# Kernel tuning notes

Measured on AMD Instinct MI355X. Metric: run time of the kernel, lower is better.

Reference implementation:

```python
import jax, jax.numpy as jnp
import numpy as np

B, L, T = 256, 1024, 128

def setup_inputs() -> dict:
    key = jax.random.key(0)
    k1, k2, k3, k4 = jax.random.split(key, 4)
    inputs = jax.random.normal(k1, (B, L, T), dtype=jnp.float32)
    tag_indices = jax.random.randint(k2, (B, L), 0, T, dtype=jnp.int64)
    sequence_lengths = jax.random.randint(k3, (B,), 1, L + 1, dtype=jnp.int64)
    # xavier-ish scale for transitions
    transition_params = jax.random.normal(k4, (T, T), dtype=jnp.float32) * (2.0 / (T + T)) ** 0.5
    return {"inputs": inputs, "tag_indices": tag_indices,
            "sequence_lengths": sequence_lengths, "transition_params": transition_params}

def _crf_log_likelihood(inputs, tag_indices, sequence_lengths, transition_params):
    b, l, t = inputs.shape
    mask = (jnp.arange(l)[None, :] < sequence_lengths[:, None]).astype(inputs.dtype)  # [B,L]

    # --- unary score: sum_t inputs[b, t, tag[b,t]] over valid t ---
    unary = jnp.take_along_axis(inputs, tag_indices[:, :, None], axis=2)[:, :, 0]  # [B,L]
    unary_score = jnp.sum(unary * mask, axis=1)

    # --- binary score: sum_t trans[tag[t], tag[t+1]] masked by mask[:,1:] ---
    trans_sc = transition_params[tag_indices[:, :-1], tag_indices[:, 1:]]  # [B,L-1]
    binary_score = jnp.sum(trans_sc * mask[:, 1:], axis=1)
    sequence_scores = unary_score + binary_score

    # --- log normalizer via forward algorithm (log-space scan) ---
    first = inputs[:, 0]                               # [B,T]
    rest = jnp.transpose(inputs[:, 1:], (1, 0, 2))     # [L-1,B,T]

    def step(state, inp_t):
        # state: [B,T] previous alphas; transition broadcast: [B,T_prev,T_next]
        new = inp_t + jax.nn.logsumexp(state[:, :, None] + transition_params[None], axis=1)
        return new, new

    _, alphas = jax.lax.scan(step, first, rest)        # [L-1,B,T]
    # original indexes all_alphas at max(0, seq_len - 2)
    idx = jnp.clip(sequence_lengths - 2, 0, l - 2)
    final_alphas = alphas[idx, jnp.arange(b)]          # [B,T]
    log_norm = jax.nn.logsumexp(final_alphas, axis=1)
    log_norm = jnp.where(sequence_lengths <= 0, jnp.zeros_like(log_norm), log_norm)

    return sequence_scores - log_norm

def reference(inputs, tag_indices, sequence_lengths, transition_params):
    return _crf_log_likelihood(inputs, tag_indices, sequence_lengths, transition_params)
```

## Files before the change

kernel.cpp:

```cpp
#include <hip/hip_runtime.h>


#define B_   256
#define LL   1024
#define TT   128
#define NBLK 16
#define L2E  1.4426950408889634f
#define LN2f 0.6931471805599453f

typedef __attribute__((ext_vector_type(8))) short bf16x8;
typedef __attribute__((ext_vector_type(4))) float f32x4;
union bfrw { unsigned w[4]; bf16x8 v; };

__device__ __forceinline__ unsigned bfround(float x) {
    unsigned u = __float_as_uint(x);
    return u + 0x7fffu + ((u >> 16) & 1u);
}
__device__ __forceinline__ unsigned pack2(float lo, float hi) {
#if __has_builtin(__builtin_amdgcn_cvt_pk_bf16_f32)
    auto p = __builtin_amdgcn_cvt_pk_bf16_f32(lo, hi);
    unsigned w; __builtin_memcpy(&w, &p, 4); return w;
#else
    return __builtin_amdgcn_perm(bfround(hi), bfround(lo), 0x07060302);
#endif
}
__device__ __forceinline__ void lds_barrier() {
    asm volatile("s_waitcnt lgkmcnt(0)\n\ts_barrier" ::: "memory");
}


template<bool FWD, int PH>
__device__ __forceinline__ void phase(int t, float& Dacc,
                                      float4 (&up)[4][2],
                                      const bf16x8 (&af)[2][4],
                                      bf16x8& bs,
                                      short* fset, float* sb2,
                                      const float* pu,
                                      float* cl, float* dc,
                                      int o0, int o1, int o2, int ws,
                                      int cb, int tfin, int W4, int q, int b)
{
    constexpr int CUR  = PH & 1;
    constexpr int NXT  = CUR ^ 1;
    constexpr int SLOT = FWD ? ((1 + PH) & 3) : ((3 - PH) & 3);

    bf16x8 bo0 = *(const bf16x8*)(fset + CUR * 2048 + o0);
    bf16x8 bo1 = *(const bf16x8*)(fset + CUR * 2048 + o1);
    bf16x8 bo2 = *(const bf16x8*)(fset + CUR * 2048 + o2);
    float sprev = sb2[CUR * 16 + b];

    f32x4 ae0, ae1, ao0, ao1;
    ae0 = __builtin_amdgcn_mfma_f32_16x16x32_bf16(af[0][0], bs,  (f32x4){0.f,0.f,0.f,0.f}, 0, 0, 0);
    ae1 = __builtin_amdgcn_mfma_f32_16x16x32_bf16(af[1][0], bs,  (f32x4){0.f,0.f,0.f,0.f}, 0, 0, 0);
    ao0 = __builtin_amdgcn_mfma_f32_16x16x32_bf16(af[0][1], bo0, (f32x4){0.f,0.f,0.f,0.f}, 0, 0, 0);
    ao1 = __builtin_amdgcn_mfma_f32_16x16x32_bf16(af[1][1], bo0, (f32x4){0.f,0.f,0.f,0.f}, 0, 0, 0);
    ae0 = __builtin_amdgcn_mfma_f32_16x16x32_bf16(af[0][2], bo1, ae0, 0, 0, 0);
    ae1 = __builtin_amdgcn_mfma_f32_16x16x32_bf16(af[1][2], bo1, ae1, 0, 0, 0);
    ao0 = __builtin_amdgcn_mfma_f32_16x16x32_bf16(af[0][3], bo2, ao0, 0, 0, 0);
    ao1 = __builtin_amdgcn_mfma_f32_16x16x32_bf16(af[1][3], bo2, ao1, 0, 0, 0);

    float ex[2][4];
    #pragma unroll
    for (int m = 0; m < 2; ++m) {
        float4 v = up[SLOT][m];
        ex[m][0] = __builtin_amdgcn_exp2f(v.x * L2E);
        ex[m][1] = __builtin_amdgcn_exp2f(v.y * L2E);
        ex[m][2] = __builtin_amdgcn_exp2f(v.z * L2E);
        ex[m][3] = __builtin_amdgcn_exp2f(v.w * L2E);
    }
    {
        int tp = FWD ? (t + 4) : (t - 5);
        tp = tp < 0 ? 0 : (tp > LL - 1 ? LL - 1 : tp);
        const float* pt = pu + (size_t)tp * TT;
        up[SLOT][0] = *(const float4*)(pt);
        up[SLOT][1] = *(const float4*)(pt + 16);
    }

    float ci = __builtin_amdgcn_rcpf(sprev);
    float lg = __builtin_amdgcn_logf(sprev);
    bool inj = (!FWD) && (tfin == t - 1);
    float cis  = inj ? 0.f : ci;
    float injf = inj ? 1.f : 0.f;
    Dacc = inj ? 0.f : (Dacc + lg);

    f32x4 a0 = ae0 + ao0;
    f32x4 a1 = ae1 + ao1;

    float rv[2][4];
    #pragma unroll
    for (int r = 0; r < 4; ++r) {
        rv[0][r] = cis * a0[r] + injf;
        rv[1][r] = cis * a1[r] + injf;
    }

    if (!FWD) {
        bool cap = (cb == t - 1) && (cb != tfin);
        if (__any(cap)) {
            if (cap) {
                float4 c0 = {rv[0][0], rv[0][1], rv[0][2], rv[0][3]};
                float4 c1 = {rv[1][0], rv[1][1], rv[1][2], rv[1][3]};
                *(float4*)(cl + b * TT + 32 * W4 + q * 4)      = c0;
                *(float4*)(cl + b * TT + 32 * W4 + 16 + q * 4) = c1;
                if (W4 == 0 && q == 0) dc[b] = Dacc;
            }
        }
    }

    float ov[2][4];
    #pragma unroll
    for (int r = 0; r < 4; ++r) {
        ov[0][r] = ex[0][r] * rv[0][r];
        ov[1][r] = ex[1][r] * rv[1][r];
    }

    if (FWD) {
        bool cap = (cb == t);
        if (__any(cap)) {
            if (cap) {
                float4 c0 = {ov[0][0], ov[0][1], ov[0][2], ov[0][3]};
                float4 c1 = {ov[1][0], ov[1][1], ov[1][2], ov[1][3]};
                *(float4*)(cl + b * TT + 32 * W4 + q * 4)      = c0;
                *(float4*)(cl + b * TT + 32 * W4 + 16 + q * 4) = c1;
                if (W4 == 0 && q == 0) dc[b] = Dacc;
            }
        }
    }

    if (W4 == 0 && q == 0) sb2[NXT * 16 + b] = a0[0];

    bfrw pk;
    pk.w[0] = pack2(ov[0][0], ov[0][1]);
    pk.w[1] = pack2(ov[0][2], ov[0][3]);
    pk.w[2] = pack2(ov[1][0], ov[1][1]);
    pk.w[3] = pack2(ov[1][2], ov[1][3]);
    bs = pk.v;
    *(bf16x8*)(fset + NXT * 2048 + ws) = pk.v;

    lds_barrier();
}

__launch_bounds__(512, 1)
__global__ void crf_scan(const float* __restrict__ inputs,
                         const int*   __restrict__ tags,
                         const int*   __restrict__ slens,
                         const float* __restrict__ trans,
                         float* __restrict__ qcap, float* __restrict__ rcap,
                         float* __restrict__ dqv,  float* __restrict__ drv,
                         int* __restrict__ perm, float* __restrict__ scorebuf)
{
    __shared__ __align__(16) short fragls[2][2][4][64 * 8];
    __shared__ __align__(16) float capl[2][16][TT];
    __shared__ float dcap[2][16];
    __shared__ float sbuf[2][2][16];
    __shared__ float ssb[8];
    __shared__ int keys[B_];

    const int tid = threadIdx.x;

    if (blockIdx.x >= NBLK) {
        const int sbid = blockIdx.x - NBLK;
        const int lane = tid & 63, w = tid >> 6;
        #pragma unroll 1
        for (int bi = 0; bi < 4; ++bi) {
            const int b = sbid * 4 + bi;
            const int slen = slens[b];
            const float* inb  = inputs + (size_t)b * LL * TT;
            const int*   tagb = tags + b * LL;
            float sc = 0.f;
            for (int t = tid; t < slen; t += 512) {
                int tg = tagb[t];
                float v = inb[(size_t)t * TT + tg];
                if (t >= 1) v += trans[tagb[t - 1] * TT + tg];
                sc += v;
            }
            #pragma unroll
            for (int off = 32; off > 0; off >>= 1) sc += __shfl_xor(sc, off, 64);
            if (lane == 0) ssb[w] = sc;
            __syncthreads();
            if (tid == 0) scorebuf[b] = ssb[0] + ssb[1] + ssb[2] + ssb[3]
                                      + ssb[4] + ssb[5] + ssb[6] + ssb[7];
            __syncthreads();
        }
        return;
    }

    const int g = blockIdx.x;

    if (tid < 256) keys[tid] = slens[tid] * 256 + tid;
    __syncthreads();
    for (int k = 2; k <= B_; k <<= 1) {
        for (int s = k >> 1; s > 0; s >>= 1) {
            if (tid < 256) {
                int ixj = tid ^ s;
                if (ixj > tid) {
                    int a = keys[tid], b2 = keys[ixj];
                    bool asc = ((tid & k) == 0);
                    if ((a > b2) == asc) { keys[tid] = b2; keys[ixj] = a; }
                }
            }
            __syncthreads();
        }
    }
    if (tid < 16) perm[g * 16 + tid] = keys[g * 16 + tid] & 255;

    const int set  = tid >> 8;
    const bool isf = (set == 0);
    const int lane = tid & 63;
    const int W4   = __builtin_amdgcn_readfirstlane((tid >> 6) & 3);
    const int q    = lane >> 4;
    const int b    = lane & 15;

    const int key = keys[g * 16 + b];
    const int ob  = key & 255;
    const int sl  = key >> 8;
    int tfin = sl - 1; if (tfin < 1) tfin = 1;

    int tmax = tfin;
    #pragma unroll
    for (int o = 1; o < 16; o <<= 1) {
        int c2 = __shfl_xor(tmax, o, 16); tmax = c2 > tmax ? c2 : tmax;
    }
    tmax = __builtin_amdgcn_readfirstlane(tmax);

    const int C  = (tmax + 4) >> 1;
    const int cb = tfin < C ? tfin : C;

    int cmax = cb, cmin = cb;
    #pragma unroll
    for (int o = 1; o < 16; o <<= 1) {
        int a = __shfl_xor(cmax, o, 16); cmax = a > cmax ? a : cmax;
        int b2 = __shfl_xor(cmin, o, 16); cmin = b2 < cmin ? b2 : cmin;
    }
    cmax = __builtin_amdgcn_readfirstlane(cmax);
    cmin = __builtin_amdgcn_readfirstlane(cmin);

    const int tb0 = (tmax + 4) & ~3;
    const int nif = (cmax + 3) >> 2;
    const int nib = (tb0 - cmin + 3) >> 2;
    const int NS  = nif > nib ? nif : nib;

    const int c1 = (W4 == 0) ? 1 : 0;
    const int c2 = (W4 <= 1) ? 2 : 1;
    const int c3 = (W4 <= 2) ? 3 : 2;
    const int o0 = (c1 * 64 + lane) * 8;
    const int o1 = (c2 * 64 + lane) * 8;
    const int o2 = (c3 * 64 + lane) * 8;
    const int ws = (W4 * 64 + lane) * 8;

    bf16x8 af[2][4];
    #pragma unroll
    for (int m = 0; m < 2; ++m) {
        const int j = 32 * W4 + 16 * m + b;
        #pragma unroll
        for (int i = 0; i < 4; ++i) {
            const int c = (i == 0) ? W4 : (i == 1) ? c1 : (i == 2) ? c2 : c3;
            #pragma unroll
            for (int jj = 0; jj < 8; ++jj) {
                int k = 32 * c + 16 * (jj >> 2) + 4 * q + (jj & 3);
                int idx = isf ? (k * TT + j) : (j * TT + k);
                float ev = __builtin_amdgcn_exp2f(trans[idx] * L2E);
                af[m][i][jj] = (short)(bfround(ev) >> 16);
            }
        }
    }

    short* fset = &fragls[set][0][0][0];
    float* sb2  = &sbuf[set][0][0];
    float* cl   = &capl[set][0][0];
    float* dc   = &dcap[set][0];

    const float* pu = inputs + (size_t)ob * LL * TT + 32 * W4 + q * 4;
    float Dacc = 0.f;
    float4 up[4][2];
    bf16x8 bs;

    if (W4 == 0 && lane < 16) sb2[lane] = 1.0f;

    if (isf) {
        float q0[2][4];
        #pragma unroll
        for (int m = 0; m < 2; ++m) {
            float4 v = *(const float4*)(pu + m * 16);
            q0[m][0] = __builtin_amdgcn_exp2f(v.x * L2E);
            q0[m][1] = __builtin_amdgcn_exp2f(v.y * L2E);
            q0[m][2] = __builtin_amdgcn_exp2f(v.z * L2E);
            q0[m][3] = __builtin_amdgcn_exp2f(v.w * L2E);
        }
        bfrw pk;
        pk.w[0] = pack2(q0[0][0], q0[0][1]);
        pk.w[1] = pack2(q0[0][2], q0[0][3]);
        pk.w[2] = pack2(q0[1][0], q0[1][1]);
        pk.w[3] = pack2(q0[1][2], q0[1][3]);
        bs = pk.v;
        *(bf16x8*)(fset + ws) = pk.v;

        #pragma unroll
        for (int s = 1; s <= 4; ++s) {
            up[s & 3][0] = *(const float4*)(pu + (size_t)s * TT);
            up[s & 3][1] = *(const float4*)(pu + (size_t)s * TT + 16);
        }
    } else {
        bfrw pk;
        pk.w[0] = pk.w[1] = pk.w[2] = pk.w[3] = 0x3F803F80u;
        bs = pk.v;
        *(bf16x8*)(fset + ws) = pk.v;
        if (cb == tfin) {
            float4 one4 = {1.f, 1.f, 1.f, 1.f};
            *(float4*)(cl + b * TT + 32 * W4 + q * 4)      = one4;
            *(float4*)(cl + b * TT + 32 * W4 + 16 + q * 4) = one4;
            if (W4 == 0 && q == 0) dc[b] = 0.f;
        }
        #pragma unroll
        for (int ph = 0; ph < 4; ++ph) {
            int ui = tb0 - 1 - ph;
            ui = ui > LL - 1 ? LL - 1 : (ui < 0 ? 0 : ui);
            up[(3 - ph) & 3][0] = *(const float4*)(pu + (size_t)ui * TT);
            up[(3 - ph) & 3][1] = *(const float4*)(pu + (size_t)ui * TT + 16);
        }
    }
    __syncthreads();

    if (isf) {
        for (int i = 0; i < NS; ++i) {
            const int tb = 1 + 4 * i;
            phase<true,0>(tb+0, Dacc, up, af, bs, fset, sb2, pu, cl, dc, o0,o1,o2,ws, cb, tfin, W4, q, b);
            phase<true,1>(tb+1, Dacc, up, af, bs, fset, sb2, pu, cl, dc, o0,o1,o2,ws, cb, tfin, W4, q, b);
            phase<true,2>(tb+2, Dacc, up, af, bs, fset, sb2, pu, cl, dc, o0,o1,o2,ws, cb, tfin, W4, q, b);
            phase<true,3>(tb+3, Dacc, up, af, bs, fset, sb2, pu, cl, dc, o0,o1,o2,ws, cb, tfin, W4, q, b);
        }
    } else {
        for (int i = 0; i < NS; ++i) {
            const int tb = tb0 - 4 * i;
            phase<false,0>(tb-0, Dacc, up, af, bs, fset, sb2, pu, cl, dc, o0,o1,o2,ws, cb, tfin, W4, q, b);
            phase<false,1>(tb-1, Dacc, up, af, bs, fset, sb2, pu, cl, dc, o0,o1,o2,ws, cb, tfin, W4, q, b);
            phase<false,2>(tb-2, Dacc, up, af, bs, fset, sb2, pu, cl, dc, o0,o1,o2,ws, cb, tfin, W4, q, b);
            phase<false,3>(tb-3, Dacc, up, af, bs, fset, sb2, pu, cl, dc, o0,o1,o2,ws, cb, tfin, W4, q, b);
        }
    }

    float* gout = isf ? qcap : rcap;
    const int ltid = tid & 255;
    #pragma unroll
    for (int i = 0; i < 2; ++i) {
        float4 v = *(const float4*)(cl + i * 1024 + ltid * 4);
        *(float4*)(gout + (size_t)g * 16 * TT + i * 1024 + ltid * 4) = v;
    }
    if (ltid < 16) (isf ? dqv : drv)[g * 16 + ltid] = dc[ltid];
}

__global__ void crf_comb(const float* __restrict__ qcap, const float* __restrict__ rcap,
                         const float* __restrict__ dqv, const float* __restrict__ drv,
                         const int* __restrict__ perm, const float* __restrict__ scorebuf,
                         float* __restrict__ out) {
    const int tid = threadIdx.x;
    const int r16 = tid >> 4, part = tid & 15;
    const int rank = blockIdx.x * 16 + r16;
    const float* qc = qcap + rank * TT + part * 8;
    const float* rc = rcap + rank * TT + part * 8;
    float4 a0 = *(const float4*)(qc);
    float4 a1 = *(const float4*)(qc + 4);
    float4 b0 = *(const float4*)(rc);
    float4 b1 = *(const float4*)(rc + 4);
    float s = a0.x*b0.x + a0.y*b0.y + a0.z*b0.z + a0.w*b0.w
            + a1.x*b1.x + a1.y*b1.y + a1.z*b1.z + a1.w*b1.w;
    #pragma unroll
    for (int o = 1; o < 16; o <<= 1) s += __shfl_xor(s, o, 16);
    if (part == 0) {
        int ob = perm[rank];
        float logZ = LN2f * (__builtin_amdgcn_logf(s) + dqv[rank] + drv[rank]);
        out[ob] = scorebuf[ob] - logZ;
    }
}

extern "C" void kernel_launch(void* const* d_in, const int* in_sizes, int n_in,
                              void* d_out, int out_size, void* d_ws, size_t ws_size,
                              hipStream_t stream) {
    const float* inputs = (const float*)d_in[0];
    const int*   tags   = (const int*)d_in[1];
    const int*   slens  = (const int*)d_in[2];
    const float* trans  = (const float*)d_in[3];
    float* out = (float*)d_out;

    float* qcap = (float*)d_ws;
    float* rcap = qcap + 32768;
    float* dqv  = rcap + 32768;
    float* drv  = dqv + 256;
    int*   perm = (int*)(drv + 256);
    float* scorebuf = (float*)(perm + 256);

    crf_scan<<<NBLK + 64, 512, 0, stream>>>(inputs, tags, slens, trans,
                                            qcap, rcap, dqv, drv, perm, scorebuf);
    crf_comb<<<NBLK, 256, 0, stream>>>(qcap, rcap, dqv, drv, perm, scorebuf, out);
}
```

Before: 465.9 us.

## Replace per-step block barriers with per-direction LDS counter flag synchronization

Swaps the workgroup-wide s_barrier after every scan step for per-wave LDS step counters. Each wave publishes its step number and spins until the other three waves of the same direction reach the previous step. This decouples the forward and backward halves of the block, so each runs only its own step count (nif or nib) instead of the common maximum. The risks are spin-polling overhead and memory-ordering hazards: the double-buffered fragments are guarded only by waits on the previous step, so a fast wave may overwrite a buffer a slower wave is still reading.

```diff
diff --git a/kernel.cpp b/kernel.cpp
--- a/kernel.cpp
+++ b/kernel.cpp
@@ -24,25 +24,38 @@
     return __builtin_amdgcn_perm(bfround(hi), bfround(lo), 0x07060302);
 #endif
 }
-__device__ __forceinline__ void lds_barrier() {
-    asm volatile("s_waitcnt lgkmcnt(0)\n\ts_barrier" ::: "memory");
-}
 
 
 template<bool FWD, int PH>
-__device__ __forceinline__ void phase(int t, float& Dacc,
+__device__ __forceinline__ void phase(int t, int s, float& Dacc,
                                       float4 (&up)[4][2],
                                       const bf16x8 (&af)[2][4],
                                       bf16x8& bs,
-                                      short* fset, float* sb2,
+                                      short* fset, float* sb2, int* cnts,
+                                      int4& cpre,
                                       const float* pu,
                                       float* cl, float* dc,
                                       int o0, int o1, int o2, int ws,
-                                      int cb, int tfin, int W4, int q, int b)
+                                      int cb, int tfin, int W4, int q, int b,
+                                      int lane)
 {
     constexpr int CUR  = PH & 1;
     constexpr int NXT  = CUR ^ 1;
     constexpr int SLOT = FWD ? ((1 + PH) & 3) : ((3 - PH) & 3);
+
+    {
+        const int need = s - 1;
+        int mn0 = cpre.x < cpre.y ? cpre.x : cpre.y;
+        int mn1 = cpre.z < cpre.w ? cpre.z : cpre.w;
+        int mn  = mn0 < mn1 ? mn0 : mn1;
+        while (mn < need) {
+            volatile const int* vc = (volatile const int*)cnts;
+            int a0 = vc[0], a1 = vc[1], a2 = vc[2], a3 = vc[3];
+            mn0 = a0 < a1 ? a0 : a1;
+            mn1 = a2 < a3 ? a2 : a3;
+            mn  = mn0 < mn1 ? mn0 : mn1;
+        }
+    }
 
     bf16x8 bo0 = *(const bf16x8*)(fset + CUR * 2048 + o0);
     bf16x8 bo1 = *(const bf16x8*)(fset + CUR * 2048 + o1);
@@ -136,7 +149,12 @@
     bs = pk.v;
     *(bf16x8*)(fset + NXT * 2048 + ws) = pk.v;
 
-    lds_barrier();
+    asm volatile("s_waitcnt lgkmcnt(0)" ::: "memory");
+    if (lane == 0) *(volatile int*)(cnts + W4) = s;
+    {
+        volatile const int* vc = (volatile const int*)cnts;
+        cpre.x = vc[0]; cpre.y = vc[1]; cpre.z = vc[2]; cpre.w = vc[3];
+    }
 }
 
 __launch_bounds__(512, 1)
@@ -150,6 +168,7 @@
 {
     __shared__ __align__(16) short fragls[2][2][4][64 * 8];
     __shared__ __align__(16) float capl[2][16][TT];
+    __shared__ __align__(16) int cnt[2][4];
     __shared__ float dcap[2][16];
     __shared__ float sbuf[2][2][16];
     __shared__ float ssb[8];
@@ -187,6 +206,7 @@
     const int g = blockIdx.x;
 
     if (tid < 256) keys[tid] = slens[tid] * 256 + tid;
+    if (tid < 8) cnt[tid >> 2][tid & 3] = 0;
     __syncthreads();
     for (int k = 2; k <= B_; k <<= 1) {
         for (int s = k >> 1; s > 0; s >>= 1) {
@@ -237,7 +257,6 @@
     const int tb0 = (tmax + 4) & ~3;
     const int nif = (cmax + 3) >> 2;
     const int nib = (tb0 - cmin + 3) >> 2;
-    const int NS  = nif > nib ? nif : nib;
 
     const int c1 = (W4 == 0) ? 1 : 0;
     const int c2 = (W4 <= 1) ? 2 : 1;
@@ -268,11 +287,13 @@
     float* sb2  = &sbuf[set][0][0];
     float* cl   = &capl[set][0][0];
     float* dc   = &dcap[set][0];
+    int*   cnts = &cnt[set][0];
 
     const float* pu = inputs + (size_t)ob * LL * TT + 32 * W4 + q * 4;
     float Dacc = 0.f;
     float4 up[4][2];
     bf16x8 bs;
+    int4 cpre = {0, 0, 0, 0};
 
     if (W4 == 0 && lane < 16) sb2[lane] = 1.0f;
 
@@ -321,22 +342,25 @@
     __syncthreads();
 
     if (isf) {
-        for (int i = 0; i < NS; ++i) {
+        for (int i = 0; i < nif; ++i) {
             const int tb = 1 + 4 * i;
-            phase<true,0>(tb+0, Dacc, up, af, bs, fset, sb2, pu, cl, dc, o0,o1,o2,ws, cb, tfin, W4, q, b);
-            phase<true,1>(tb+1, Dacc, up, af, bs, fset, sb2, pu, cl, dc, o0,o1,o2,ws, cb, tfin, W4, q, b);
-            phase<true,2>(tb+2, Dacc, up, af, bs, fset, sb2, pu, cl, dc, o0,o1,o2,ws, cb, tfin, W4, q, b);
-            phase<true,3>(tb+3, Dacc, up, af, bs, fset, sb2, pu, cl, dc, o0,o1,o2,ws, cb, tfin, W4, q, b);
+            phase<true,0>(tb+0, tb+0, Dacc, up, af, bs, fset, sb2, cnts, cpre, pu, cl, dc, o0,o1,o2,ws, cb, tfin, W4, q, b, lane);
+            phase<true,1>(tb+1, tb+1, Dacc, up, af, bs, fset, sb2, cnts, cpre, pu, cl, dc, o0,o1,o2,ws, cb, tfin, W4, q, b, lane);
+            phase<true,2>(tb+2, tb+2, Dacc, up, af, bs, fset, sb2, cnts, cpre, pu, cl, dc, o0,o1,o2,ws, cb, tfin, W4, q, b, lane);
+            phase<true,3>(tb+3, tb+3, Dacc, up, af, bs, fset, sb2, cnts, cpre, pu, cl, dc, o0,o1,o2,ws, cb, tfin, W4, q, b, lane);
         }
     } else {
-        for (int i = 0; i < NS; ++i) {
+        for (int i = 0; i < nib; ++i) {
             const int tb = tb0 - 4 * i;
-            phase<false,0>(tb-0, Dacc, up, af, bs, fset, sb2, pu, cl, dc, o0,o1,o2,ws, cb, tfin, W4, q, b);
-            phase<false,1>(tb-1, Dacc, up, af, bs, fset, sb2, pu, cl, dc, o0,o1,o2,ws, cb, tfin, W4, q, b);
-            phase<false,2>(tb-2, Dacc, up, af, bs, fset, sb2, pu, cl, dc, o0,o1,o2,ws, cb, tfin, W4, q, b);
-            phase<false,3>(tb-3, Dacc, up, af, bs, fset, sb2, pu, cl, dc, o0,o1,o2,ws, cb, tfin, W4, q, b);
-        }
-    }
+            const int s0 = 4 * i + 1;
+            phase<false,0>(tb-0, s0+0, Dacc, up, af, bs, fset, sb2, cnts, cpre, pu, cl, dc, o0,o1,o2,ws, cb, tfin, W4, q, b, lane);
+            phase<false,1>(tb-1, s0+1, Dacc, up, af, bs, fset, sb2, cnts, cpre, pu, cl, dc, o0,o1,o2,ws, cb, tfin, W4, q, b, lane);
+            phase<false,2>(tb-2, s0+2, Dacc, up, af, bs, fset, sb2, cnts, cpre, pu, cl, dc, o0,o1,o2,ws, cb, tfin, W4, q, b, lane);
+            phase<false,3>(tb-3, s0+3, Dacc, up, af, bs, fset, sb2, cnts, cpre, pu, cl, dc, o0,o1,o2,ws, cb, tfin, W4, q, b, lane);
+        }
+    }
+
+    __syncthreads();
 
     float* gout = isf ? qcap : rcap;
     const int ltid = tid & 255;
```

New measurement: 567.6 us. 21.8% more time.

## Split forward and backward scan sets into separate 256-thread blocks

Applied to the files above, without the earlier changes.

The forward and backward half-scans used to share one 512-thread block with a shared LDS barrier. They now run as separate 256-thread blocks, twice as many, each with its own loop bound (cmax for forward, cmin for backward) instead of a common NS. This removes the coupling where each half waited at barriers for the other and ran extra iterations to match the longer half. The cost is a duplicated slen sort in every block and more blocks to launch.

```diff
diff --git a/kernel.cpp b/kernel.cpp
--- a/kernel.cpp
+++ b/kernel.cpp
@@ -34,20 +34,20 @@
                                       float4 (&up)[4][2],
                                       const bf16x8 (&af)[2][4],
                                       bf16x8& bs,
-                                      short* fset, float* sb2,
+                                      short* fragls, float* sbuf,
                                       const float* pu,
-                                      float* cl, float* dc,
+                                      float* capl, float* dcap,
                                       int o0, int o1, int o2, int ws,
-                                      int cb, int tfin, int W4, int q, int b)
+                                      int cb, int tfin, int W, int q, int b)
 {
     constexpr int CUR  = PH & 1;
     constexpr int NXT  = CUR ^ 1;
     constexpr int SLOT = FWD ? ((1 + PH) & 3) : ((3 - PH) & 3);
 
-    bf16x8 bo0 = *(const bf16x8*)(fset + CUR * 2048 + o0);
-    bf16x8 bo1 = *(const bf16x8*)(fset + CUR * 2048 + o1);
-    bf16x8 bo2 = *(const bf16x8*)(fset + CUR * 2048 + o2);
-    float sprev = sb2[CUR * 16 + b];
+    bf16x8 bo0 = *(const bf16x8*)(fragls + CUR * 2048 + o0);
+    bf16x8 bo1 = *(const bf16x8*)(fragls + CUR * 2048 + o1);
+    bf16x8 bo2 = *(const bf16x8*)(fragls + CUR * 2048 + o2);
+    float sprev = sbuf[CUR * 16 + b];
 
     f32x4 ae0, ae1, ao0, ao1;
     ae0 = __builtin_amdgcn_mfma_f32_16x16x32_bf16(af[0][0], bs,  (f32x4){0.f,0.f,0.f,0.f}, 0, 0, 0);
@@ -99,9 +99,9 @@
             if (cap) {
                 float4 c0 = {rv[0][0], rv[0][1], rv[0][2], rv[0][3]};
                 float4 c1 = {rv[1][0], rv[1][1], rv[1][2], rv[1][3]};
-                *(float4*)(cl + b * TT + 32 * W4 + q * 4)      = c0;
-                *(float4*)(cl + b * TT + 32 * W4 + 16 + q * 4) = c1;
-                if (W4 == 0 && q == 0) dc[b] = Dacc;
+                *(float4*)(capl + b * TT + 32 * W + q * 4)      = c0;
+                *(float4*)(capl + b * TT + 32 * W + 16 + q * 4) = c1;
+                if (W == 0 && q == 0) dcap[b] = Dacc;
             }
         }
     }
@@ -119,14 +119,14 @@
             if (cap) {
                 float4 c0 = {ov[0][0], ov[0][1], ov[0][2], ov[0][3]};
                 float4 c1 = {ov[1][0], ov[1][1], ov[1][2], ov[1][3]};
-                *(float4*)(cl + b * TT + 32 * W4 + q * 4)      = c0;
-                *(float4*)(cl + b * TT + 32 * W4 + 16 + q * 4) = c1;
-                if (W4 == 0 && q == 0) dc[b] = Dacc;
-            }
-        }
-    }
-
-    if (W4 == 0 && q == 0) sb2[NXT * 16 + b] = a0[0];
+                *(float4*)(capl + b * TT + 32 * W + q * 4)      = c0;
+                *(float4*)(capl + b * TT + 32 * W + 16 + q * 4) = c1;
+                if (W == 0 && q == 0) dcap[b] = Dacc;
+            }
+        }
+    }
+
+    if (W == 0 && q == 0) sbuf[NXT * 16 + b] = a0[0];
 
     bfrw pk;
     pk.w[0] = pack2(ov[0][0], ov[0][1]);
@@ -134,12 +134,12 @@
     pk.w[2] = pack2(ov[1][0], ov[1][1]);
     pk.w[3] = pack2(ov[1][2], ov[1][3]);
     bs = pk.v;
-    *(bf16x8*)(fset + NXT * 2048 + ws) = pk.v;
+    *(bf16x8*)(fragls + NXT * 2048 + ws) = pk.v;
 
     lds_barrier();
 }
 
-__launch_bounds__(512, 1)
+__launch_bounds__(256, 1)
 __global__ void crf_scan(const float* __restrict__ inputs,
                          const int*   __restrict__ tags,
                          const int*   __restrict__ slens,
@@ -148,17 +148,17 @@
                          float* __restrict__ dqv,  float* __restrict__ drv,
                          int* __restrict__ perm, float* __restrict__ scorebuf)
 {
-    __shared__ __align__(16) short fragls[2][2][4][64 * 8];
-    __shared__ __align__(16) float capl[2][16][TT];
-    __shared__ float dcap[2][16];
-    __shared__ float sbuf[2][2][16];
-    __shared__ float ssb[8];
+    __shared__ __align__(16) short fragls[2 * 4 * 64 * 8];
+    __shared__ __align__(16) float capl[16 * TT];
+    __shared__ float dcap[16];
+    __shared__ float sbuf[2 * 16];
+    __shared__ float ssb[4];
     __shared__ int keys[B_];
 
     const int tid = threadIdx.x;
 
-    if (blockIdx.x >= NBLK) {
-        const int sbid = blockIdx.x - NBLK;
+    if (blockIdx.x >= 2 * NBLK) {
+        const int sbid = blockIdx.x - 2 * NBLK;
         const int lane = tid & 63, w = tid >> 6;
         #pragma unroll 1
         for (int bi = 0; bi < 4; ++bi) {
@@ -167,7 +167,7 @@
             const float* inb  = inputs + (size_t)b * LL * TT;
             const int*   tagb = tags + b * LL;
             float sc = 0.f;
-            for (int t = tid; t < slen; t += 512) {
+            for (int t = tid; t < slen; t += 256) {
                 int tg = tagb[t];
                 float v = inb[(size_t)t * TT + tg];
                 if (t >= 1) v += trans[tagb[t - 1] * TT + tg];
@@ -177,36 +177,32 @@
             for (int off = 32; off > 0; off >>= 1) sc += __shfl_xor(sc, off, 64);
             if (lane == 0) ssb[w] = sc;
             __syncthreads();
-            if (tid == 0) scorebuf[b] = ssb[0] + ssb[1] + ssb[2] + ssb[3]
-                                      + ssb[4] + ssb[5] + ssb[6] + ssb[7];
+            if (tid == 0) scorebuf[b] = ssb[0] + ssb[1] + ssb[2] + ssb[3];
             __syncthreads();
         }
         return;
     }
 
-    const int g = blockIdx.x;
-
-    if (tid < 256) keys[tid] = slens[tid] * 256 + tid;
+    keys[tid] = slens[tid] * 256 + tid;
     __syncthreads();
     for (int k = 2; k <= B_; k <<= 1) {
         for (int s = k >> 1; s > 0; s >>= 1) {
-            if (tid < 256) {
-                int ixj = tid ^ s;
-                if (ixj > tid) {
-                    int a = keys[tid], b2 = keys[ixj];
-                    bool asc = ((tid & k) == 0);
-                    if ((a > b2) == asc) { keys[tid] = b2; keys[ixj] = a; }
-                }
+            int ixj = tid ^ s;
+            if (ixj > tid) {
+                int a = keys[tid], b2 = keys[ixj];
+                bool asc = ((tid & k) == 0);
+                if ((a > b2) == asc) { keys[tid] = b2; keys[ixj] = a; }
             }
             __syncthreads();
         }
     }
-    if (tid < 16) perm[g * 16 + tid] = keys[g * 16 + tid] & 255;
-
-    const int set  = tid >> 8;
-    const bool isf = (set == 0);
+
+    const bool isf = (blockIdx.x < NBLK);
+    const int g    = isf ? blockIdx.x : blockIdx.x - NBLK;
+    if (isf && tid < 16) perm[g * 16 + tid] = keys[g * 16 + tid] & 255;
+
     const int lane = tid & 63;
-    const int W4   = __builtin_amdgcn_readfirstlane((tid >> 6) & 3);
+    const int W    = __builtin_amdgcn_readfirstlane(tid >> 6);
     const int q    = lane >> 4;
     const int b    = lane & 15;
 
@@ -235,25 +231,22 @@
     cmin = __builtin_amdgcn_readfirstlane(cmin);
 
     const int tb0 = (tmax + 4) & ~3;
-    const int nif = (cmax + 3) >> 2;
-    const int nib = (tb0 - cmin + 3) >> 2;
-    const int NS  = nif > nib ? nif : nib;
-
-    const int c1 = (W4 == 0) ? 1 : 0;
-    const int c2 = (W4 <= 1) ? 2 : 1;
-    const int c3 = (W4 <= 2) ? 3 : 2;
+
+    const int c1 = (W == 0) ? 1 : 0;
+    const int c2 = (W <= 1) ? 2 : 1;
+    const int c3 = (W <= 2) ? 3 : 2;
     const int o0 = (c1 * 64 + lane) * 8;
     const int o1 = (c2 * 64 + lane) * 8;
     const int o2 = (c3 * 64 + lane) * 8;
-    const int ws = (W4 * 64 + lane) * 8;
+    const int ws = (W  * 64 + lane) * 8;
 
     bf16x8 af[2][4];
     #pragma unroll
     for (int m = 0; m < 2; ++m) {
-        const int j = 32 * W4 + 16 * m + b;
+        const int j = 32 * W + 16 * m + b;
         #pragma unroll
         for (int i = 0; i < 4; ++i) {
-            const int c = (i == 0) ? W4 : (i == 1) ? c1 : (i == 2) ? c2 : c3;
+            const int c = (i == 0) ? W : (i == 1) ? c1 : (i == 2) ? c2 : c3;
             #pragma unroll
             for (int jj = 0; jj < 8; ++jj) {
                 int k = 32 * c + 16 * (jj >> 2) + 4 * q + (jj & 3);
@@ -264,17 +257,12 @@
         }
     }
 
-    short* fset = &fragls[set][0][0][0];
-    float* sb2  = &sbuf[set][0][0];
-    float* cl   = &capl[set][0][0];
-    float* dc   = &dcap[set][0];
-
-    const float* pu = inputs + (size_t)ob * LL * TT + 32 * W4 + q * 4;
+    const float* pu = inputs + (size_t)ob * LL * TT + 32 * W + q * 4;
     float Dacc = 0.f;
     float4 up[4][2];
     bf16x8 bs;
 
-    if (W4 == 0 && lane < 16) sb2[lane] = 1.0f;
+    if (tid < 16) sbuf[tid] = 1.0f;
 
     if (isf) {
         float q0[2][4];
@@ -292,23 +280,31 @@
         pk.w[2] = pack2(q0[1][0], q0[1][1]);
         pk.w[3] = pack2(q0[1][2], q0[1][3]);
         bs = pk.v;
-        *(bf16x8*)(fset + ws) = pk.v;
+        *(bf16x8*)(fragls + ws) = pk.v;
 
         #pragma unroll
         for (int s = 1; s <= 4; ++s) {
             up[s & 3][0] = *(const float4*)(pu + (size_t)s * TT);
             up[s & 3][1] = *(const float4*)(pu + (size_t)s * TT + 16);
         }
+        __syncthreads();
+
+        for (int tb = 1; tb <= cmax; tb += 4) {
+            phase<true,0>(tb+0, Dacc, up, af, bs, fragls, sbuf, pu, capl, dcap, o0,o1,o2,ws, cb, tfin, W, q, b);
+            phase<true,1>(tb+1, Dacc, up, af, bs, fragls, sbuf, pu, capl, dcap, o0,o1,o2,ws, cb, tfin, W, q, b);
+            phase<true,2>(tb+2, Dacc, up, af, bs, fragls, sbuf, pu, capl, dcap, o0,o1,o2,ws, cb, tfin, W, q, b);
+            phase<true,3>(tb+3, Dacc, up, af, bs, fragls, sbuf, pu, capl, dcap, o0,o1,o2,ws, cb, tfin, W, q, b);
+        }
     } else {
         bfrw pk;
         pk.w[0] = pk.w[1] = pk.w[2] = pk.w[3] = 0x3F803F80u;
         bs = pk.v;
-        *(bf16x8*)(fset + ws) = pk.v;
+        *(bf16x8*)(fragls + ws) = pk.v;
         if (cb == tfin) {
             float4 one4 = {1.f, 1.f, 1.f, 1.f};
-            *(float4*)(cl + b * TT + 32 * W4 + q * 4)      = one4;
-            *(float4*)(cl + b * TT + 32 * W4 + 16 + q * 4) = one4;
-            if (W4 == 0 && q == 0) dc[b] = 0.f;
+            *(float4*)(capl + b * TT + 32 * W + q * 4)      = one4;
+            *(float4*)(capl + b * TT + 32 * W + 16 + q * 4) = one4;
+            if (W == 0 && q == 0) dcap[b] = 0.f;
         }
         #pragma unroll
         for (int ph = 0; ph < 4; ++ph) {
@@ -317,35 +313,23 @@
             up[(3 - ph) & 3][0] = *(const float4*)(pu + (size_t)ui * TT);
             up[(3 - ph) & 3][1] = *(const float4*)(pu + (size_t)ui * TT + 16);
         }
-    }
-    __syncthreads();
-
-    if (isf) {
-        for (int i = 0; i < NS; ++i) {
-            const int tb = 1 + 4 * i;
-            phase<true,0>(tb+0, Dacc, up, af, bs, fset, sb2, pu, cl, dc, o0,o1,o2,ws, cb, tfin, W4, q, b);
-            phase<true,1>(tb+1, Dacc, up, af, bs, fset, sb2, pu, cl, dc, o0,o1,o2,ws, cb, tfin, W4, q, b);
-            phase<true,2>(tb+2, Dacc, up, af, bs, fset, sb2, pu, cl, dc, o0,o1,o2,ws, cb, tfin, W4, q, b);
-            phase<true,3>(tb+3, Dacc, up, af, bs, fset, sb2, pu, cl, dc, o0,o1,o2,ws, cb, tfin, W4, q, b);
-        }
-    } else {
-        for (int i = 0; i < NS; ++i) {
-            const int tb = tb0 - 4 * i;
-            phase<false,0>(tb-0, Dacc, up, af, bs, fset, sb2, pu, cl, dc, o0,o1,o2,ws, cb, tfin, W4, q, b);
-            phase<false,1>(tb-1, Dacc, up, af, bs, fset, sb2, pu, cl, dc, o0,o1,o2,ws, cb, tfin, W4, q, b);
-            phase<false,2>(tb-2, Dacc, up, af, bs, fset, sb2, pu, cl, dc, o0,o1,o2,ws, cb, tfin, W4, q, b);
-            phase<false,3>(tb-3, Dacc, up, af, bs, fset, sb2, pu, cl, dc, o0,o1,o2,ws, cb, tfin, W4, q, b);
+        __syncthreads();
+
+        for (int tb = tb0; tb > cmin; tb -= 4) {
+            phase<false,0>(tb-0, Dacc, up, af, bs, fragls, sbuf, pu, capl, dcap, o0,o1,o2,ws, cb, tfin, W, q, b);
+            phase<false,1>(tb-1, Dacc, up, af, bs, fragls, sbuf, pu, capl, dcap, o0,o1,o2,ws, cb, tfin, W, q, b);
+            phase<false,2>(tb-2, Dacc, up, af, bs, fragls, sbuf, pu, capl, dcap, o0,o1,o2,ws, cb, tfin, W, q, b);
+            phase<false,3>(tb-3, Dacc, up, af, bs, fragls, sbuf, pu, capl, dcap, o0,o1,o2,ws, cb, tfin, W, q, b);
         }
     }
 
     float* gout = isf ? qcap : rcap;
-    const int ltid = tid & 255;
     #pragma unroll
     for (int i = 0; i < 2; ++i) {
-        float4 v = *(const float4*)(cl + i * 1024 + ltid * 4);
-        *(float4*)(gout + (size_t)g * 16 * TT + i * 1024 + ltid * 4) = v;
-    }
-    if (ltid < 16) (isf ? dqv : drv)[g * 16 + ltid] = dc[ltid];
+        float4 v = *(const float4*)(capl + i * 1024 + tid * 4);
+        *(float4*)(gout + (size_t)g * 16 * TT + i * 1024 + tid * 4) = v;
+    }
+    if (tid < 16) (isf ? dqv : drv)[g * 16 + tid] = dcap[tid];
 }
 
 __global__ void crf_comb(const float* __restrict__ qcap, const float* __restrict__ rcap,
@@ -388,7 +372,7 @@
     int*   perm = (int*)(drv + 256);
     float* scorebuf = (float*)(perm + 256);
 
-    crf_scan<<<NBLK + 64, 512, 0, stream>>>(inputs, tags, slens, trans,
-                                            qcap, rcap, dqv, drv, perm, scorebuf);
+    crf_scan<<<2 * NBLK + 64, 256, 0, stream>>>(inputs, tags, slens, trans,
+                                                qcap, rcap, dqv, drv, perm, scorebuf);
     crf_comb<<<NBLK, 256, 0, stream>>>(qcap, rcap, dqv, drv, perm, scorebuf, out);
 }
```

Measured after the change: 411.3 us. -11.7%, faster.
